# Kernel tuning notes

Measured on AMD Instinct MI355X. Metric: run time of the kernel, lower is better.

## Reference

```python
import jax, jax.numpy as jnp
import numpy as np

B, S, D, UNITS = 32, 4096, 512, 512


def setup_inputs() -> dict:
    key = jax.random.key(0)
    ks = jax.random.split(key, 8)
    scale = 0.05
    return {
        "query": jax.random.normal(ks[0], (B, D), dtype=jnp.float32),
        "values": jax.random.normal(ks[1], (B, S, D), dtype=jnp.float32),
        "W1": jax.random.normal(ks[2], (D, UNITS), dtype=jnp.float32) * scale,
        "b1": jnp.zeros((UNITS,), dtype=jnp.float32),
        "W2": jax.random.normal(ks[3], (D, UNITS), dtype=jnp.float32) * scale,
        "b2": jnp.zeros((UNITS,), dtype=jnp.float32),
        "V": jax.random.normal(ks[4], (UNITS, 1), dtype=jnp.float32) * scale,
        "bv": jnp.zeros((1,), dtype=jnp.float32),
    }


def reference(query, values, W1, b1, W2, b2, V, bv):
    # values: [B, S, D], query: [B, D]
    proj_v = jnp.einsum("bsd,du->bsu", values, W1) + b1          # [B, S, U]
    proj_q = (query @ W2 + b2)[:, None, :]                        # [B, 1, U]
    score = jnp.tanh(proj_v + proj_q) @ V + bv                    # [B, S, 1]
    attention_weights = jax.nn.softmax(score, axis=1)             # [B, S, 1]
    context_vector = jnp.sum(attention_weights * values, axis=1)  # [B, D]
    return (context_vector, attention_weights)
```

## Files before the change

### kernel.cpp

```cpp
#include <hip/hip_runtime.h>

#define NB 32
#define NS 4096
#define ND 512
#define NU 512

typedef __attribute__((ext_vector_type(8))) __bf16 bf16x8;
typedef __attribute__((ext_vector_type(8))) short short8;
typedef __attribute__((ext_vector_type(4))) float f32x4;

union Cvt8 { __bf16 h[8]; short8 s8; };

__device__ __forceinline__ float fast_tanh(float x) {
  float e = __expf(2.0f * x);
  return 1.0f - __fdividef(2.0f, e + 1.0f);
}

__global__ void pack_w1_kernel(const float* __restrict__ W1, __bf16* __restrict__ W1f) {
  int idx = blockIdx.x * 256 + threadIdx.x;
  int l  = idx & 63;
  int ct = (idx >> 6) & 31;
  int ks = idx >> 11;
  int col   = ct * 16 + (l & 15);
  int kbase = ks * 32 + (l >> 4) * 8;
  Cvt8 u;
#pragma unroll
  for (int j = 0; j < 8; ++j) u.h[j] = (__bf16)W1[(size_t)(kbase + j) * NU + col];
  *reinterpret_cast<short8*>(W1f + (size_t)idx * 8) = u.s8;
}

__global__ void proj_query_kernel(const float* __restrict__ query, const float* __restrict__ W2,
                                  const float* __restrict__ b2, const float* __restrict__ b1,
                                  float* __restrict__ pq) {
  int b = blockIdx.y;
  int u = blockIdx.x * 256 + threadIdx.x;
  const float* q = query + (size_t)b * ND;
  float acc = b2[u] + b1[u];
  for (int k = 0; k < ND; ++k) acc += q[k] * W2[(size_t)k * NU + u];
  pq[(size_t)b * NU + u] = acc;
}

__device__ __forceinline__ void stage_chunk(const float* __restrict__ vbase, char* base,
                                            int tid, int kh, int chunk) {
  int idx = chunk * 512 + tid;
  int row = idx >> 5;
  int c8  = idx & 31;
  const float4* src = reinterpret_cast<const float4*>(vbase + (size_t)row * ND + kh * 256 + c8 * 8);
  float4 f0 = src[0], f1 = src[1];
  Cvt8 u;
  u.h[0] = (__bf16)f0.x; u.h[1] = (__bf16)f0.y; u.h[2] = (__bf16)f0.z; u.h[3] = (__bf16)f0.w;
  u.h[4] = (__bf16)f1.x; u.h[5] = (__bf16)f1.y; u.h[6] = (__bf16)f1.z; u.h[7] = (__bf16)f1.w;
  int boff = row * 512 + ((c8 * 16) ^ ((row & 7) << 4));
  *reinterpret_cast<short8*>(base + boff) = u.s8;
}

__global__ __launch_bounds__(512, 4)
void score_kernel(const float* __restrict__ values, const __bf16* __restrict__ W1f,
                  const float* __restrict__ pq, const float* __restrict__ V,
                  float* __restrict__ scoreW) {
  __shared__ char ldsb[65536];
  char* buf0 = ldsb;
  char* buf1 = ldsb + 32768;

  int bid = blockIdx.x;
  int b = bid >> 6;
  int s0 = (bid & 63) * 64;
  int tid = threadIdx.x;
  int l = tid & 63;
  int w = tid >> 6;
  int lane_col = l & 15;
  int lane_k8  = l >> 4;

  const float* vbase = values + ((size_t)b * NS + s0) * ND;
  const __bf16* wptr = W1f + ((size_t)(w * 4) * 64 + l) * 8;

#pragma unroll
  for (int c = 0; c < 4; ++c) stage_chunk(vbase, buf0, tid, 0, c);
  __syncthreads();

  f32x4 acc[4][4];
#pragma unroll
  for (int rf = 0; rf < 4; ++rf)
#pragma unroll
    for (int cf = 0; cf < 4; ++cf) acc[rf][cf] = (f32x4){0.f, 0.f, 0.f, 0.f};

#pragma unroll
  for (int kh = 0; kh < 2; ++kh) {
    char* rbuf = (kh == 0) ? buf0 : buf1;
#pragma unroll
    for (int ks = 0; ks < 8; ++ks) {
      if (kh == 0 && ks < 4) stage_chunk(vbase, buf1, tid, 1, ks);
      bf16x8 a[4];
      int kbyte = ks * 64 + lane_k8 * 16;
#pragma unroll
      for (int rf = 0; rf < 4; ++rf) {
        int row = rf * 16 + lane_col;
        a[rf] = *reinterpret_cast<const bf16x8*>(rbuf + row * 512 + (kbyte ^ ((row & 7) << 4)));
      }
      int kg = kh * 8 + ks;
      bf16x8 bb[4];
#pragma unroll
      for (int cf = 0; cf < 4; ++cf)
        bb[cf] = *reinterpret_cast<const bf16x8*>(wptr + (size_t)kg * 16384 + cf * 512);
#pragma unroll
      for (int cf = 0; cf < 4; ++cf)
#pragma unroll
        for (int rf = 0; rf < 4; ++rf)
          acc[rf][cf] = __builtin_amdgcn_mfma_f32_16x16x32_bf16(a[rf], bb[cf], acc[rf][cf], 0, 0, 0);
    }
    if (kh == 0) __syncthreads();
  }

  float partial[4][4];
#pragma unroll
  for (int rf = 0; rf < 4; ++rf)
#pragma unroll
    for (int r = 0; r < 4; ++r) partial[rf][r] = 0.f;

  const float* pqb = pq + (size_t)b * NU;
#pragma unroll
  for (int cf = 0; cf < 4; ++cf) {
    int col = w * 64 + cf * 16 + lane_col;
    float pqv = pqb[col];
    float Vv  = V[col];
#pragma unroll
    for (int rf = 0; rf < 4; ++rf)
#pragma unroll
      for (int r = 0; r < 4; ++r)
        partial[rf][r] += fast_tanh(acc[rf][cf][r] + pqv) * Vv;
  }

#pragma unroll
  for (int off = 1; off < 16; off <<= 1)
#pragma unroll
    for (int rf = 0; rf < 4; ++rf)
#pragma unroll
      for (int r = 0; r < 4; ++r) partial[rf][r] += __shfl_xor(partial[rf][r], off);

  float* sbuf = (float*)ldsb;
  if (lane_col == 0) {
#pragma unroll
    for (int rf = 0; rf < 4; ++rf)
#pragma unroll
      for (int r = 0; r < 4; ++r)
        sbuf[w * 64 + rf * 16 + lane_k8 * 4 + r] = partial[rf][r];
  }
  __syncthreads();
  if (tid < 64) {
    float sc = 0.f;
#pragma unroll
    for (int wv = 0; wv < 8; ++wv) sc += sbuf[wv * 64 + tid];
    scoreW[(size_t)b * NS + s0 + tid] = sc;
  }
}

__global__ void softmax_kernel(const float* __restrict__ scoreW, float* __restrict__ attn) {
  int b = blockIdx.x, tid = threadIdx.x;
  __shared__ float sred[8];
  const float* sc = scoreW + (size_t)b * NS;
  float m = -3.0e38f;
  for (int s = tid; s < NS; s += 256) m = fmaxf(m, sc[s]);
#pragma unroll
  for (int off = 1; off < 64; off <<= 1) m = fmaxf(m, __shfl_xor(m, off));
  if ((tid & 63) == 0) sred[tid >> 6] = m;
  __syncthreads();
  m = fmaxf(fmaxf(sred[0], sred[1]), fmaxf(sred[2], sred[3]));
  float sum = 0.f;
  for (int s = tid; s < NS; s += 256) sum += __expf(sc[s] - m);
#pragma unroll
  for (int off = 1; off < 64; off <<= 1) sum += __shfl_xor(sum, off);
  if ((tid & 63) == 0) sred[4 + (tid >> 6)] = sum;
  __syncthreads();
  float inv = 1.f / (sred[4] + sred[5] + sred[6] + sred[7]);
  float* ab = attn + (size_t)b * NS;
  for (int s = tid; s < NS; s += 256) ab[s] = __expf(sc[s] - m) * inv;
}

__global__ void context_partial_kernel(const float* __restrict__ values,
                                       const float* __restrict__ attn,
                                       float* __restrict__ ctxpart) {
  int blk = blockIdx.x;
  int b = blk >> 4, c = blk & 15;
  int tid = threadIdx.x;
  int t2 = tid & 127;
  int sg = tid >> 7;
  const float* vb = values + ((size_t)b * NS + c * 256) * ND;
  const float* ab = attn + (size_t)b * NS + c * 256;
  f32x4 acc = {0.f, 0.f, 0.f, 0.f};
  for (int s = sg; s < 256; s += 2) {
    float wv = ab[s];
    f32x4 v = *reinterpret_cast<const f32x4*>(vb + (size_t)s * ND + t2 * 4);
    acc += v * wv;
  }
  __shared__ f32x4 red[128];
  if (sg == 1) red[t2] = acc;
  __syncthreads();
  if (sg == 0) {
    acc += red[t2];
    *reinterpret_cast<f32x4*>(ctxpart + (size_t)blk * ND + t2 * 4) = acc;
  }
}

__global__ void context_reduce_kernel(const float* __restrict__ ctxpart, float* __restrict__ ctx) {
  int b = blockIdx.x, tid = threadIdx.x;
  f32x4 acc = {0.f, 0.f, 0.f, 0.f};
  for (int c = 0; c < 16; ++c)
    acc += *reinterpret_cast<const f32x4*>(ctxpart + (size_t)(b * 16 + c) * ND + tid * 4);
  *reinterpret_cast<f32x4*>(ctx + (size_t)b * ND + tid * 4) = acc;
}

extern "C" void kernel_launch(void* const* d_in, const int* in_sizes, int n_in,
                              void* d_out, int out_size, void* d_ws, size_t ws_size,
                              hipStream_t stream) {
  const float* query  = (const float*)d_in[0];
  const float* values = (const float*)d_in[1];
  const float* W1     = (const float*)d_in[2];
  const float* b1     = (const float*)d_in[3];
  const float* W2     = (const float*)d_in[4];
  const float* b2     = (const float*)d_in[5];
  const float* V      = (const float*)d_in[6];

  float* ctx_out  = (float*)d_out;
  float* attn_out = ctx_out + NB * ND;

  char* ws = (char*)d_ws;
  __bf16* W1f    = (__bf16*)ws;
  float*  pq     = (float*)(ws + 524288);
  float*  scoreW = (float*)(ws + 589824);
  float*  ctxp   = (float*)(ws + 1114112);

  hipLaunchKernelGGL(pack_w1_kernel,        dim3(128),     dim3(256), 0, stream, W1, W1f);
  hipLaunchKernelGGL(proj_query_kernel,     dim3(2, NB),   dim3(256), 0, stream, query, W2, b2, b1, pq);
  hipLaunchKernelGGL(score_kernel,          dim3(2048),    dim3(512), 0, stream, values, W1f, pq, V, scoreW);
  hipLaunchKernelGGL(softmax_kernel,        dim3(NB),      dim3(256), 0, stream, scoreW, attn_out);
  hipLaunchKernelGGL(context_partial_kernel,dim3(NB * 16), dim3(256), 0, stream, values, attn_out, ctxp);
  hipLaunchKernelGGL(context_reduce_kernel, dim3(NB),      dim3(128), 0, stream, ctxp, ctx_out);
}
```

Measured before the change: 210.1 us.

## Make score kernel persistent over four row tiles with register-staged software pipeline

```diff
diff --git a/kernel.cpp b/kernel.cpp
--- a/kernel.cpp
+++ b/kernel.cpp
@@ -40,117 +40,166 @@
   pq[(size_t)b * NU + u] = acc;
 }
 
-__device__ __forceinline__ void stage_chunk(const float* __restrict__ vbase, char* base,
-                                            int tid, int kh, int chunk) {
-  int idx = chunk * 512 + tid;
-  int row = idx >> 5;
-  int c8  = idx & 31;
-  const float4* src = reinterpret_cast<const float4*>(vbase + (size_t)row * ND + kh * 256 + c8 * 8);
-  float4 f0 = src[0], f1 = src[1];
-  Cvt8 u;
-  u.h[0] = (__bf16)f0.x; u.h[1] = (__bf16)f0.y; u.h[2] = (__bf16)f0.z; u.h[3] = (__bf16)f0.w;
-  u.h[4] = (__bf16)f1.x; u.h[5] = (__bf16)f1.y; u.h[6] = (__bf16)f1.z; u.h[7] = (__bf16)f1.w;
-  int boff = row * 512 + ((c8 * 16) ^ ((row & 7) << 4));
-  *reinterpret_cast<short8*>(base + boff) = u.s8;
-}
-
 __global__ __launch_bounds__(512, 4)
 void score_kernel(const float* __restrict__ values, const __bf16* __restrict__ W1f,
                   const float* __restrict__ pq, const float* __restrict__ V,
                   float* __restrict__ scoreW) {
-  __shared__ char ldsb[65536];
+  __shared__ __align__(16) char ldsb[67584];
   char* buf0 = ldsb;
   char* buf1 = ldsb + 32768;
-
-  int bid = blockIdx.x;
-  int b = bid >> 6;
-  int s0 = (bid & 63) * 64;
+  float* sbuf = (float*)(ldsb + 65536);
+
+  int g = blockIdx.x;
+  int b = g >> 4;
+  int s0 = (g & 15) * 256;
   int tid = threadIdx.x;
   int l = tid & 63;
   int w = tid >> 6;
   int lane_col = l & 15;
   int lane_k8  = l >> 4;
 
-  const float* vbase = values + ((size_t)b * NS + s0) * ND;
-  const __bf16* wptr = W1f + ((size_t)(w * 4) * 64 + l) * 8;
-
-#pragma unroll
-  for (int c = 0; c < 4; ++c) stage_chunk(vbase, buf0, tid, 0, c);
-  __syncthreads();
-
-  f32x4 acc[4][4];
-#pragma unroll
-  for (int rf = 0; rf < 4; ++rf)
-#pragma unroll
-    for (int cf = 0; cf < 4; ++cf) acc[rf][cf] = (f32x4){0.f, 0.f, 0.f, 0.f};
-
-#pragma unroll
-  for (int kh = 0; kh < 2; ++kh) {
-    char* rbuf = (kh == 0) ? buf0 : buf1;
-#pragma unroll
-    for (int ks = 0; ks < 8; ++ks) {
-      if (kh == 0 && ks < 4) stage_chunk(vbase, buf1, tid, 1, ks);
-      bf16x8 a[4];
-      int kbyte = ks * 64 + lane_k8 * 16;
-#pragma unroll
-      for (int rf = 0; rf < 4; ++rf) {
-        int row = rf * 16 + lane_col;
-        a[rf] = *reinterpret_cast<const bf16x8*>(rbuf + row * 512 + (kbyte ^ ((row & 7) << 4)));
-      }
-      int kg = kh * 8 + ks;
-      bf16x8 bb[4];
-#pragma unroll
-      for (int cf = 0; cf < 4; ++cf)
-        bb[cf] = *reinterpret_cast<const bf16x8*>(wptr + (size_t)kg * 16384 + cf * 512);
-#pragma unroll
-      for (int cf = 0; cf < 4; ++cf)
-#pragma unroll
-        for (int rf = 0; rf < 4; ++rf)
-          acc[rf][cf] = __builtin_amdgcn_mfma_f32_16x16x32_bf16(a[rf], bb[cf], acc[rf][cf], 0, 0, 0);
-    }
-    if (kh == 0) __syncthreads();
-  }
-
-  float partial[4][4];
-#pragma unroll
-  for (int rf = 0; rf < 4; ++rf)
-#pragma unroll
-    for (int r = 0; r < 4; ++r) partial[rf][r] = 0.f;
-
-  const float* pqb = pq + (size_t)b * NU;
+  float pqv[4], Vv[4];
 #pragma unroll
   for (int cf = 0; cf < 4; ++cf) {
     int col = w * 64 + cf * 16 + lane_col;
-    float pqv = pqb[col];
-    float Vv  = V[col];
+    pqv[cf] = pq[(size_t)b * NU + col];
+    Vv[cf]  = V[col];
+  }
+
+  const float* vb0 = values + ((size_t)b * NS + s0) * ND;
+  const __bf16* wptr = W1f + ((size_t)(w * 4) * 64 + l) * 8;
+
+  float4 st[2];
+  float4 st2[2];
+
+  auto loadu = [&](float4* s, int tile, int kh, int c) {
+    int idx = c * 512 + tid;
+    int row = idx >> 5, c8 = idx & 31;
+    const float4* p = reinterpret_cast<const float4*>(
+        vb0 + (size_t)(tile * 64 + row) * ND + kh * 256 + c8 * 8);
+    s[0] = p[0]; s[1] = p[1];
+  };
+  auto writeu = [&](const float4* s, char* dbuf, int c) {
+    int idx = c * 512 + tid;
+    int row = idx >> 5, c8 = idx & 31;
+    Cvt8 u;
+    u.h[0] = (__bf16)s[0].x; u.h[1] = (__bf16)s[0].y; u.h[2] = (__bf16)s[0].z; u.h[3] = (__bf16)s[0].w;
+    u.h[4] = (__bf16)s[1].x; u.h[5] = (__bf16)s[1].y; u.h[6] = (__bf16)s[1].z; u.h[7] = (__bf16)s[1].w;
+    int boff = row * 512 + ((c8 * 16) ^ ((row & 7) << 4));
+    *reinterpret_cast<short8*>(dbuf + boff) = u.s8;
+  };
+
+  f32x4 acc[4][4];
+#pragma unroll
+  for (int rf = 0; rf < 4; ++rf)
+#pragma unroll
+    for (int cf = 0; cf < 4; ++cf) acc[rf][cf] = (f32x4){0.f, 0.f, 0.f, 0.f};
+
+#pragma unroll
+  for (int c = 0; c < 4; c += 2) {
+    loadu(st, 0, 0, c); loadu(st2, 0, 0, c + 1);
+    writeu(st, buf0, c); writeu(st2, buf0, c + 1);
+  }
+
+  auto ksstep = [&](char* rbuf, int kg, int ks) {
+    bf16x8 a[4];
+    int kbyte = ks * 64 + lane_k8 * 16;
+#pragma unroll
+    for (int rf = 0; rf < 4; ++rf) {
+      int row = rf * 16 + lane_col;
+      a[rf] = *reinterpret_cast<const bf16x8*>(rbuf + row * 512 + (kbyte ^ ((row & 7) << 4)));
+    }
+    bf16x8 bb[4];
+#pragma unroll
+    for (int cf = 0; cf < 4; ++cf)
+      bb[cf] = *reinterpret_cast<const bf16x8*>(wptr + (size_t)kg * 16384 + cf * 512);
+    __builtin_amdgcn_s_setprio(1);
+#pragma unroll
+    for (int cf = 0; cf < 4; ++cf)
+#pragma unroll
+      for (int rf = 0; rf < 4; ++rf)
+        acc[rf][cf] = __builtin_amdgcn_mfma_f32_16x16x32_bf16(a[rf], bb[cf], acc[rf][cf], 0, 0, 0);
+    __builtin_amdgcn_s_setprio(0);
+  };
+
+  auto epilogue = [&](int tile) {
+    float partial[4][4];
 #pragma unroll
     for (int rf = 0; rf < 4; ++rf)
 #pragma unroll
-      for (int r = 0; r < 4; ++r)
-        partial[rf][r] += fast_tanh(acc[rf][cf][r] + pqv) * Vv;
-  }
-
-#pragma unroll
-  for (int off = 1; off < 16; off <<= 1)
+      for (int r = 0; r < 4; ++r) partial[rf][r] = 0.f;
+#pragma unroll
+    for (int cf = 0; cf < 4; ++cf)
+#pragma unroll
+      for (int rf = 0; rf < 4; ++rf)
+#pragma unroll
+        for (int r = 0; r < 4; ++r)
+          partial[rf][r] += fast_tanh(acc[rf][cf][r] + pqv[cf]) * Vv[cf];
+#pragma unroll
+    for (int off = 1; off < 16; off <<= 1)
+#pragma unroll
+      for (int rf = 0; rf < 4; ++rf)
+#pragma unroll
+        for (int r = 0; r < 4; ++r) partial[rf][r] += __shfl_xor(partial[rf][r], off);
+    if (lane_col == 0) {
+#pragma unroll
+      for (int rf = 0; rf < 4; ++rf)
+#pragma unroll
+        for (int r = 0; r < 4; ++r)
+          sbuf[w * 64 + rf * 16 + lane_k8 * 4 + r] = partial[rf][r];
+    }
+    __syncthreads();
+    if (tid < 64) {
+      float sc = 0.f;
+#pragma unroll
+      for (int wv = 0; wv < 8; ++wv) sc += sbuf[wv * 64 + tid];
+      scoreW[(size_t)b * NS + s0 + tile * 64 + tid] = sc;
+    }
 #pragma unroll
     for (int rf = 0; rf < 4; ++rf)
 #pragma unroll
-      for (int r = 0; r < 4; ++r) partial[rf][r] += __shfl_xor(partial[rf][r], off);
-
-  float* sbuf = (float*)ldsb;
-  if (lane_col == 0) {
-#pragma unroll
-    for (int rf = 0; rf < 4; ++rf)
-#pragma unroll
-      for (int r = 0; r < 4; ++r)
-        sbuf[w * 64 + rf * 16 + lane_k8 * 4 + r] = partial[rf][r];
-  }
-  __syncthreads();
-  if (tid < 64) {
-    float sc = 0.f;
-#pragma unroll
-    for (int wv = 0; wv < 8; ++wv) sc += sbuf[wv * 64 + tid];
-    scoreW[(size_t)b * NS + s0 + tid] = sc;
+      for (int cf = 0; cf < 4; ++cf) acc[rf][cf] = (f32x4){0.f, 0.f, 0.f, 0.f};
+  };
+
+  for (int hp = 0; hp < 4; ++hp) {
+    __syncthreads();
+    loadu(st, hp, 1, 0);
+    ksstep(buf0, 0, 0);
+    loadu(st2, hp, 1, 1);
+    ksstep(buf0, 1, 1);
+    writeu(st, buf1, 0);
+    ksstep(buf0, 2, 2);
+    loadu(st, hp, 1, 2);
+    ksstep(buf0, 3, 3);
+    writeu(st2, buf1, 1);
+    ksstep(buf0, 4, 4);
+    loadu(st2, hp, 1, 3);
+    ksstep(buf0, 5, 5);
+    writeu(st, buf1, 2);
+    ksstep(buf0, 6, 6);
+    ksstep(buf0, 7, 7);
+    writeu(st2, buf1, 3);
+
+    __syncthreads();
+    bool more = (hp < 3);
+    if (more) loadu(st, hp + 1, 0, 0);
+    ksstep(buf1, 8, 0);
+    if (more) loadu(st2, hp + 1, 0, 1);
+    ksstep(buf1, 9, 1);
+    if (more) writeu(st, buf0, 0);
+    ksstep(buf1, 10, 2);
+    if (more) loadu(st, hp + 1, 0, 2);
+    ksstep(buf1, 11, 3);
+    if (more) writeu(st2, buf0, 1);
+    ksstep(buf1, 12, 4);
+    if (more) loadu(st2, hp + 1, 0, 3);
+    ksstep(buf1, 13, 5);
+    if (more) writeu(st, buf0, 2);
+    ksstep(buf1, 14, 6);
+    ksstep(buf1, 15, 7);
+    if (more) writeu(st2, buf0, 3);
+
+    epilogue(hp);
   }
 }
 
@@ -231,7 +280,7 @@
 
   hipLaunchKernelGGL(pack_w1_kernel,        dim3(128),     dim3(256), 0, stream, W1, W1f);
   hipLaunchKernelGGL(proj_query_kernel,     dim3(2, NB),   dim3(256), 0, stream, query, W2, b2, b1, pq);
-  hipLaunchKernelGGL(score_kernel,          dim3(2048),    dim3(512), 0, stream, values, W1f, pq, V, scoreW);
+  hipLaunchKernelGGL(score_kernel,          dim3(512),     dim3(512), 0, stream, values, W1f, pq, V, scoreW);
   hipLaunchKernelGGL(softmax_kernel,        dim3(NB),      dim3(256), 0, stream, scoreW, attn_out);
   hipLaunchKernelGGL(context_partial_kernel,dim3(NB * 16), dim3(256), 0, stream, values, attn_out, ctxp);
   hipLaunchKernelGGL(context_reduce_kernel, dim3(NB),      dim3(128), 0, stream, ctxp, ctx_out);
```

Result: slower. 473.4 us (+125.3%).

## Stage full K in fragment-ordered LDS and split score GEMM into two column passes

Applied to the files above, without the earlier changes.

```diff
diff --git a/kernel.cpp b/kernel.cpp
--- a/kernel.cpp
+++ b/kernel.cpp
@@ -40,27 +40,12 @@
   pq[(size_t)b * NU + u] = acc;
 }
 
-__device__ __forceinline__ void stage_chunk(const float* __restrict__ vbase, char* base,
-                                            int tid, int kh, int chunk) {
-  int idx = chunk * 512 + tid;
-  int row = idx >> 5;
-  int c8  = idx & 31;
-  const float4* src = reinterpret_cast<const float4*>(vbase + (size_t)row * ND + kh * 256 + c8 * 8);
-  float4 f0 = src[0], f1 = src[1];
-  Cvt8 u;
-  u.h[0] = (__bf16)f0.x; u.h[1] = (__bf16)f0.y; u.h[2] = (__bf16)f0.z; u.h[3] = (__bf16)f0.w;
-  u.h[4] = (__bf16)f1.x; u.h[5] = (__bf16)f1.y; u.h[6] = (__bf16)f1.z; u.h[7] = (__bf16)f1.w;
-  int boff = row * 512 + ((c8 * 16) ^ ((row & 7) << 4));
-  *reinterpret_cast<short8*>(base + boff) = u.s8;
-}
-
 __global__ __launch_bounds__(512, 4)
 void score_kernel(const float* __restrict__ values, const __bf16* __restrict__ W1f,
                   const float* __restrict__ pq, const float* __restrict__ V,
                   float* __restrict__ scoreW) {
-  __shared__ char ldsb[65536];
-  char* buf0 = ldsb;
-  char* buf1 = ldsb + 32768;
+  __shared__ __align__(16) char ldsb[67584];
+  float* sbuf = (float*)(ldsb + 65536);
 
   int bid = blockIdx.x;
   int b = bid >> 6;
@@ -71,79 +56,91 @@
   int lane_col = l & 15;
   int lane_k8  = l >> 4;
 
+  float pqv[4], Vv[4];
+#pragma unroll
+  for (int nb = 0; nb < 2; ++nb)
+#pragma unroll
+    for (int cf = 0; cf < 2; ++cf) {
+      int col = nb * 256 + w * 32 + cf * 16 + lane_col;
+      pqv[nb * 2 + cf] = pq[(size_t)b * NU + col];
+      Vv[nb * 2 + cf]  = V[col];
+    }
+
   const float* vbase = values + ((size_t)b * NS + s0) * ND;
-  const __bf16* wptr = W1f + ((size_t)(w * 4) * 64 + l) * 8;
-
-#pragma unroll
-  for (int c = 0; c < 4; ++c) stage_chunk(vbase, buf0, tid, 0, c);
-  __syncthreads();
-
-  f32x4 acc[4][4];
-#pragma unroll
-  for (int rf = 0; rf < 4; ++rf)
-#pragma unroll
-    for (int cf = 0; cf < 4; ++cf) acc[rf][cf] = (f32x4){0.f, 0.f, 0.f, 0.f};
-
-#pragma unroll
-  for (int kh = 0; kh < 2; ++kh) {
-    char* rbuf = (kh == 0) ? buf0 : buf1;
-#pragma unroll
-    for (int ks = 0; ks < 8; ++ks) {
-      if (kh == 0 && ks < 4) stage_chunk(vbase, buf1, tid, 1, ks);
+
+#pragma unroll
+  for (int i = 0; i < 8; ++i) {
+    int c  = i * 512 + tid;
+    int t  = c >> 10;
+    int kg = (c >> 6) & 15;
+    int ln = c & 63;
+    int s  = t * 16 + (ln & 15);
+    int c8 = kg * 4 + (ln >> 4);
+    const float4* p = reinterpret_cast<const float4*>(vbase + (size_t)s * ND + c8 * 8);
+    float4 f0 = p[0], f1 = p[1];
+    Cvt8 u;
+    u.h[0] = (__bf16)f0.x; u.h[1] = (__bf16)f0.y; u.h[2] = (__bf16)f0.z; u.h[3] = (__bf16)f0.w;
+    u.h[4] = (__bf16)f1.x; u.h[5] = (__bf16)f1.y; u.h[6] = (__bf16)f1.z; u.h[7] = (__bf16)f1.w;
+    *reinterpret_cast<short8*>(ldsb + (size_t)c * 16) = u.s8;
+  }
+  __syncthreads();
+
+  float partial[4][4];
+#pragma unroll
+  for (int t = 0; t < 4; ++t)
+#pragma unroll
+    for (int r = 0; r < 4; ++r) partial[t][r] = 0.f;
+
+#pragma unroll
+  for (int nb = 0; nb < 2; ++nb) {
+    f32x4 acc[4][2];
+#pragma unroll
+    for (int t = 0; t < 4; ++t)
+#pragma unroll
+      for (int cf = 0; cf < 2; ++cf) acc[t][cf] = (f32x4){0.f, 0.f, 0.f, 0.f};
+
+    const __bf16* wp = W1f + ((size_t)(nb * 16 + w * 2) * 64 + l) * 8;
+
+    for (int kg = 0; kg < 16; ++kg) {
       bf16x8 a[4];
-      int kbyte = ks * 64 + lane_k8 * 16;
-#pragma unroll
-      for (int rf = 0; rf < 4; ++rf) {
-        int row = rf * 16 + lane_col;
-        a[rf] = *reinterpret_cast<const bf16x8*>(rbuf + row * 512 + (kbyte ^ ((row & 7) << 4)));
-      }
-      int kg = kh * 8 + ks;
-      bf16x8 bb[4];
-#pragma unroll
-      for (int cf = 0; cf < 4; ++cf)
-        bb[cf] = *reinterpret_cast<const bf16x8*>(wptr + (size_t)kg * 16384 + cf * 512);
-#pragma unroll
-      for (int cf = 0; cf < 4; ++cf)
-#pragma unroll
-        for (int rf = 0; rf < 4; ++rf)
-          acc[rf][cf] = __builtin_amdgcn_mfma_f32_16x16x32_bf16(a[rf], bb[cf], acc[rf][cf], 0, 0, 0);
+#pragma unroll
+      for (int t = 0; t < 4; ++t)
+        a[t] = *reinterpret_cast<const bf16x8*>(ldsb + (((t * 16 + kg) * 64 + l) << 4));
+      bf16x8 bb[2];
+#pragma unroll
+      for (int cf = 0; cf < 2; ++cf)
+        bb[cf] = *reinterpret_cast<const bf16x8*>(wp + (size_t)kg * 16384 + cf * 512);
+      __builtin_amdgcn_s_setprio(1);
+#pragma unroll
+      for (int cf = 0; cf < 2; ++cf)
+#pragma unroll
+        for (int t = 0; t < 4; ++t)
+          acc[t][cf] = __builtin_amdgcn_mfma_f32_16x16x32_bf16(a[t], bb[cf], acc[t][cf], 0, 0, 0);
+      __builtin_amdgcn_s_setprio(0);
     }
-    if (kh == 0) __syncthreads();
-  }
-
-  float partial[4][4];
-#pragma unroll
-  for (int rf = 0; rf < 4; ++rf)
-#pragma unroll
-    for (int r = 0; r < 4; ++r) partial[rf][r] = 0.f;
-
-  const float* pqb = pq + (size_t)b * NU;
-#pragma unroll
-  for (int cf = 0; cf < 4; ++cf) {
-    int col = w * 64 + cf * 16 + lane_col;
-    float pqv = pqb[col];
-    float Vv  = V[col];
-#pragma unroll
-    for (int rf = 0; rf < 4; ++rf)
+
+#pragma unroll
+    for (int cf = 0; cf < 2; ++cf)
+#pragma unroll
+      for (int t = 0; t < 4; ++t)
+#pragma unroll
+        for (int r = 0; r < 4; ++r)
+          partial[t][r] += fast_tanh(acc[t][cf][r] + pqv[nb * 2 + cf]) * Vv[nb * 2 + cf];
+  }
+
+#pragma unroll
+  for (int off = 1; off < 16; off <<= 1)
+#pragma unroll
+    for (int t = 0; t < 4; ++t)
+#pragma unroll
+      for (int r = 0; r < 4; ++r) partial[t][r] += __shfl_xor(partial[t][r], off);
+
+  if (lane_col == 0) {
+#pragma unroll
+    for (int t = 0; t < 4; ++t)
 #pragma unroll
       for (int r = 0; r < 4; ++r)
-        partial[rf][r] += fast_tanh(acc[rf][cf][r] + pqv) * Vv;
-  }
-
-#pragma unroll
-  for (int off = 1; off < 16; off <<= 1)
-#pragma unroll
-    for (int rf = 0; rf < 4; ++rf)
-#pragma unroll
-      for (int r = 0; r < 4; ++r) partial[rf][r] += __shfl_xor(partial[rf][r], off);
-
-  float* sbuf = (float*)ldsb;
-  if (lane_col == 0) {
-#pragma unroll
-    for (int rf = 0; rf < 4; ++rf)
-#pragma unroll
-      for (int r = 0; r < 4; ++r)
-        sbuf[w * 64 + rf * 16 + lane_k8 * 4 + r] = partial[rf][r];
+        sbuf[w * 64 + t * 16 + lane_k8 * 4 + r] = partial[t][r];
   }
   __syncthreads();
   if (tid < 64) {
```

After: 200.6 us. 4.5% less time.
